# Performance work log

Measured on AMD Instinct MI355X. Metric: run time of the kernel, lower is better.

## Reference

```python
import jax, jax.numpy as jnp
import numpy as np


def _gcn_conv(h, src, dst, deg_inv_sqrt, W, b, num_nodes):
    # h: [N, Fin]; transform then normalized neighbor aggregation (incl. self-loops)
    h = h @ W  # [N, Fout]
    norm = deg_inv_sqrt[src] * deg_inv_sqrt[dst]  # [E+N]
    msgs = h[src] * norm[:, None]  # gather + scale
    out = jax.ops.segment_sum(msgs, dst, num_segments=num_nodes)
    return out + b


def setup_inputs() -> dict:
    key = jax.random.key(0)
    k1, k2, k3, k4 = jax.random.split(key, 4)
    N, E, F_IN, F_HID, F_OUT = 100000, 3200000, 1433, 16, 7
    x = jax.random.normal(k1, (N, F_IN), dtype=jnp.float32)
    edge_index = jax.random.randint(k2, (2, E), 0, N, dtype=jnp.int64)
    W1 = jax.random.normal(k3, (F_IN, F_HID), dtype=jnp.float32) * (1.0 / np.sqrt(F_IN))
    b1 = jnp.zeros((F_HID,), dtype=jnp.float32)
    W2 = jax.random.normal(k4, (F_HID, F_OUT), dtype=jnp.float32) * (1.0 / np.sqrt(F_HID))
    b2 = jnp.zeros((F_OUT,), dtype=jnp.float32)
    return {"x": x, "edge_index": edge_index, "W1": W1, "b1": b1, "W2": W2, "b2": b2}


def reference(x, edge_index, W1, b1, W2, b2):
    N = x.shape[0]
    # add self-loops (PyG GCNConv default)
    loops = jnp.arange(N, dtype=edge_index.dtype)
    src = jnp.concatenate([edge_index[0], loops])
    dst = jnp.concatenate([edge_index[1], loops])
    # symmetric normalization from in-degree over self-loop-augmented edges
    deg = jax.ops.segment_sum(jnp.ones_like(dst, dtype=x.dtype), dst, num_segments=N)
    deg_inv_sqrt = jnp.where(deg > 0, jax.lax.rsqrt(deg), 0.0)
    h = _gcn_conv(x, src, dst, deg_inv_sqrt, W1, b1, N)
    h = jax.nn.relu(h)
    # dropout is identity in eval mode (deterministic reference)
    h = _gcn_conv(h, src, dst, deg_inv_sqrt, W2, b2, N)
    return jax.nn.log_softmax(h, axis=1)
```

## Files before the change

kernel.cpp:

```cpp
#include <hip/hip_runtime.h>
#include <math.h>

#define F_IN 1433
#define F_HID 16
#define F_OUT 7
#define KSPLIT 8
#define KCHUNK 192
#define CAP 128
#define NSCAT 512

__device__ __forceinline__ unsigned short f2bf(float f) {
  unsigned u = __float_as_uint(f);
  u += 0x7fffu + ((u >> 16) & 1u);
  return (unsigned short)(u >> 16);
}

__device__ __forceinline__ unsigned pk2(float a, float b) {
  return (unsigned)f2bf(a) | ((unsigned)f2bf(b) << 16);
}

__device__ __forceinline__ void upk_add(unsigned u, float& lo, float& hi) {
  lo += __uint_as_float(u << 16);
  hi += __uint_as_float(u & 0xffff0000u);
}

__global__ __launch_bounds__(256) void k_zero(int* __restrict__ cnt, int N) {
  int i = blockIdx.x * 256 + threadIdx.x;
  if (i < N) cnt[i] = 0;
}

__global__ __launch_bounds__(256) void k_fused(
    const float* __restrict__ x, const float* __restrict__ W1,
    const int* __restrict__ src, const int* __restrict__ dst,
    int* __restrict__ cnt, int* __restrict__ csr, float* __restrict__ part,
    int N, int E, int nrb) {
  const int t = threadIdx.x;
  const int b = blockIdx.x;

  if (b < NSCAT) {
    const int ne4 = (E + 3) >> 2;
    for (int i4 = b * 256 + t; i4 < ne4; i4 += NSCAT * 256) {
      const int base = i4 * 4;
      if (base + 3 < E) {
        const int4 s = *(const int4*)(src + base);
        const int4 d = *(const int4*)(dst + base);
        int r;
        r = atomicAdd(&cnt[d.x], 1); csr[((size_t)d.x << 7) + r] = s.x;
        r = atomicAdd(&cnt[d.y], 1); csr[((size_t)d.y << 7) + r] = s.y;
        r = atomicAdd(&cnt[d.z], 1); csr[((size_t)d.z << 7) + r] = s.z;
        r = atomicAdd(&cnt[d.w], 1); csr[((size_t)d.w << 7) + r] = s.w;
      } else {
        for (int k = base; k < E; ++k) {
          const int d = dst[k];
          const int r = atomicAdd(&cnt[d], 1);
          csr[((size_t)d << 7) + r] = src[k];
        }
      }
    }
    return;
  }

  __shared__ float xs[256 * 33];
  const int g = b - NSCAT;
  const int chunk = g / nrb;
  const int rb = g - chunk * nrb;
  const int row0 = rb * 256;
  const int row = row0 + t;
  const int kk = t & 31;
  const int r0 = t >> 5;
  const int cbase = chunk * KCHUNK;
  const int kend = min(cbase + KCHUNK, F_IN);

  float acc[F_HID];
#pragma unroll
  for (int j = 0; j < F_HID; ++j) acc[j] = 0.0f;

  float reg[32];
  {
    const int k = cbase + kk;
    const bool kin = (k < kend);
#pragma unroll
    for (int i = 0; i < 32; ++i) {
      const int rg = row0 + r0 + 8 * i;
      reg[i] = (kin && rg < N) ? x[(size_t)rg * F_IN + k] : 0.0f;
    }
  }

  for (int k0 = cbase; k0 < kend; k0 += 32) {
#pragma unroll
    for (int i = 0; i < 32; ++i) xs[(r0 + 8 * i) * 33 + kk] = reg[i];
    __syncthreads();
    const int kn = k0 + 32;
    if (kn < kend) {
      const int k = kn + kk;
      const bool kin = (k < kend);
#pragma unroll
      for (int i = 0; i < 32; ++i) {
        const int rg = row0 + r0 + 8 * i;
        reg[i] = (kin && rg < N) ? x[(size_t)rg * F_IN + k] : 0.0f;
      }
    }
    const int kw = min(32, kend - k0);
    const float* __restrict__ wp = W1 + (size_t)k0 * F_HID;
    if (kw == 32) {
#pragma unroll
      for (int c = 0; c < 32; ++c) {
        const float xv = xs[t * 33 + c];
#pragma unroll
        for (int j = 0; j < F_HID; ++j)
          acc[j] = fmaf(xv, wp[c * F_HID + j], acc[j]);
      }
    } else {
      for (int c = 0; c < kw; ++c) {
        const float xv = xs[t * 33 + c];
#pragma unroll
        for (int j = 0; j < F_HID; ++j)
          acc[j] = fmaf(xv, wp[c * F_HID + j], acc[j]);
      }
    }
    __syncthreads();
  }

  if (row < N) {
    float4* __restrict__ pp =
        (float4*)(part + ((size_t)chunk * N + row) * F_HID);
    pp[0] = make_float4(acc[0], acc[1], acc[2], acc[3]);
    pp[1] = make_float4(acc[4], acc[5], acc[6], acc[7]);
    pp[2] = make_float4(acc[8], acc[9], acc[10], acc[11]);
    pp[3] = make_float4(acc[12], acc[13], acc[14], acc[15]);
  }
}

__global__ __launch_bounds__(256) void k_red(const float4* __restrict__ part,
                                             const int* __restrict__ cnt,
                                             uint2* __restrict__ h1b, int N) {
  const int idx = blockIdx.x * 256 + threadIdx.x;
  if (idx >= N * 4) return;
  const int row = idx >> 2;
  const size_t stride = (size_t)N * 4;
  float4 s = part[idx];
#pragma unroll
  for (int c = 1; c < KSPLIT; ++c) {
    const float4 p = part[c * stride + idx];
    s.x += p.x; s.y += p.y; s.z += p.z; s.w += p.w;
  }
  const float sc = rsqrtf((float)(cnt[row] + 1));
  uint2 o;
  o.x = pk2(s.x * sc, s.y * sc);
  o.y = pk2(s.z * sc, s.w * sc);
  h1b[idx] = o;
}

__device__ __forceinline__ void l1_finish(float a[8], int i, int d, int lane,
                                          int p, const uint4* __restrict__ h1v,
                                          const float* __restrict__ b1,
                                          const float* __restrict__ W2,
                                          uint4* __restrict__ h2v) {
#pragma unroll
  for (int m = 2; m <= 32; m <<= 1) {
#pragma unroll
    for (int j = 0; j < 8; ++j) a[j] += __shfl_xor(a[j], m);
  }
  const uint4 v = h1v[((size_t)i << 1) + p];
  upk_add(v.x, a[0], a[1]);
  upk_add(v.y, a[2], a[3]);
  upk_add(v.z, a[4], a[5]);
  upk_add(v.w, a[6], a[7]);
  const float sd = rsqrtf((float)(d + 1));
  const float4 bl = ((const float4*)b1)[p * 2];
  const float4 bh = ((const float4*)b1)[p * 2 + 1];
  float tt[8];
  tt[0] = fmaxf(fmaf(a[0], sd, bl.x), 0.f);
  tt[1] = fmaxf(fmaf(a[1], sd, bl.y), 0.f);
  tt[2] = fmaxf(fmaf(a[2], sd, bl.z), 0.f);
  tt[3] = fmaxf(fmaf(a[3], sd, bl.w), 0.f);
  tt[4] = fmaxf(fmaf(a[4], sd, bh.x), 0.f);
  tt[5] = fmaxf(fmaf(a[5], sd, bh.y), 0.f);
  tt[6] = fmaxf(fmaf(a[6], sd, bh.z), 0.f);
  tt[7] = fmaxf(fmaf(a[7], sd, bh.w), 0.f);
  const float* __restrict__ w = W2 + p * 8 * F_OUT;
  float o[F_OUT];
#pragma unroll
  for (int j = 0; j < F_OUT; ++j) {
    o[j] = tt[0] * w[0 * F_OUT + j] + tt[1] * w[1 * F_OUT + j] +
           tt[2] * w[2 * F_OUT + j] + tt[3] * w[3 * F_OUT + j] +
           tt[4] * w[4 * F_OUT + j] + tt[5] * w[5 * F_OUT + j] +
           tt[6] * w[6 * F_OUT + j] + tt[7] * w[7 * F_OUT + j];
  }
#pragma unroll
  for (int j = 0; j < F_OUT; ++j) o[j] += __shfl_xor(o[j], 1);
  if (lane == 0) {
    uint4 r;
    r.x = pk2(o[0] * sd, o[1] * sd);
    r.y = pk2(o[2] * sd, o[3] * sd);
    r.z = pk2(o[4] * sd, o[5] * sd);
    r.w = pk2(o[6] * sd, 0.0f);
    h2v[i] = r;
  }
}

__global__ __launch_bounds__(256) void k_agg1n(
    const int* __restrict__ cnt, const int* __restrict__ csr,
    const uint4* __restrict__ h1v, const float* __restrict__ b1,
    const float* __restrict__ W2, uint4* __restrict__ h2v, int N) {
  const int lane = threadIdx.x & 63;
  const int i0 = blockIdx.x * 8 + (threadIdx.x >> 6) * 2;
  if (i0 >= N) return;
  const int i1 = i0 + 1;
  const bool has1 = (i1 < N);
  const int nb = lane >> 1;
  const int p = lane & 1;

  const int d0 = cnt[i0];
  const int d1 = has1 ? cnt[i1] : 0;
  const int* __restrict__ row0 = csr + ((size_t)i0 << 7);
  const int* __restrict__ row1 = csr + ((size_t)i1 << 7);

  float A[8], B[8];
#pragma unroll
  for (int j = 0; j < 8; ++j) { A[j] = 0.f; B[j] = 0.f; }
  const int dm = max(d0, d1);
  for (int c0 = 0; c0 < dm; c0 += 32) {
    const int c = c0 + nb;
    if (c < d0) {
      const uint4 v = h1v[((size_t)row0[c] << 1) + p];
      upk_add(v.x, A[0], A[1]); upk_add(v.y, A[2], A[3]);
      upk_add(v.z, A[4], A[5]); upk_add(v.w, A[6], A[7]);
    }
    if (c < d1) {
      const uint4 v = h1v[((size_t)row1[c] << 1) + p];
      upk_add(v.x, B[0], B[1]); upk_add(v.y, B[2], B[3]);
      upk_add(v.z, B[4], B[5]); upk_add(v.w, B[6], B[7]);
    }
  }
  l1_finish(A, i0, d0, lane, p, h1v, b1, W2, h2v);
  if (has1) l1_finish(B, i1, d1, lane, p, h1v, b1, W2, h2v);
}

__device__ __forceinline__ void l2_finish(float a[8], int i, int d, int lane,
                                          const uint4* __restrict__ h2v,
                                          const float* __restrict__ b2,
                                          float* __restrict__ out) {
#pragma unroll
  for (int m = 1; m <= 32; m <<= 1) {
#pragma unroll
    for (int j = 0; j < 7; ++j) a[j] += __shfl_xor(a[j], m);
  }
  const uint4 v = h2v[i];
  upk_add(v.x, a[0], a[1]);
  upk_add(v.y, a[2], a[3]);
  upk_add(v.z, a[4], a[5]);
  float dummy = 0.f;
  upk_add(v.w, a[6], dummy);
  if (lane == 0) {
    const float sd = rsqrtf((float)(d + 1));
    float vv[7];
#pragma unroll
    for (int j = 0; j < 7; ++j) vv[j] = fmaf(a[j], sd, b2[j]);
    float m = fmaxf(fmaxf(fmaxf(vv[0], vv[1]), fmaxf(vv[2], vv[3])),
                    fmaxf(fmaxf(vv[4], vv[5]), vv[6]));
    float sum = 0.f;
#pragma unroll
    for (int j = 0; j < 7; ++j) sum += expf(vv[j] - m);
    const float l = m + logf(sum);
    float* __restrict__ op = out + (size_t)i * F_OUT;
#pragma unroll
    for (int j = 0; j < 7; ++j) op[j] = vv[j] - l;
  }
}

__global__ __launch_bounds__(256) void k_agg2n(const int* __restrict__ cnt,
                                               const int* __restrict__ csr,
                                               const uint4* __restrict__ h2v,
                                               const float* __restrict__ b2,
                                               float* __restrict__ out, int N) {
  const int lane = threadIdx.x & 63;
  const int i0 = blockIdx.x * 8 + (threadIdx.x >> 6) * 2;
  if (i0 >= N) return;
  const int i1 = i0 + 1;
  const bool has1 = (i1 < N);

  const int d0 = cnt[i0];
  const int d1 = has1 ? cnt[i1] : 0;
  const int* __restrict__ row0 = csr + ((size_t)i0 << 7);
  const int* __restrict__ row1 = csr + ((size_t)i1 << 7);

  float A[8], B[8];
#pragma unroll
  for (int j = 0; j < 8; ++j) { A[j] = 0.f; B[j] = 0.f; }
  const int dm = max(d0, d1);
  for (int c0 = 0; c0 < dm; c0 += 64) {
    const int c = c0 + lane;
    if (c < d0) {
      const uint4 v = h2v[row0[c]];
      upk_add(v.x, A[0], A[1]); upk_add(v.y, A[2], A[3]);
      upk_add(v.z, A[4], A[5]); upk_add(v.w, A[6], A[7]);
    }
    if (c < d1) {
      const uint4 v = h2v[row1[c]];
      upk_add(v.x, B[0], B[1]); upk_add(v.y, B[2], B[3]);
      upk_add(v.z, B[4], B[5]); upk_add(v.w, B[6], B[7]);
    }
  }
  l2_finish(A, i0, d0, lane, h2v, b2, out);
  if (has1) l2_finish(B, i1, d1, lane, h2v, b2, out);
}

extern "C" void kernel_launch(void* const* d_in, const int* in_sizes, int n_in,
                              void* d_out, int out_size, void* d_ws,
                              size_t ws_size, hipStream_t stream) {
  const float* x = (const float*)d_in[0];
  const int* ei = (const int*)d_in[1];
  const float* W1 = (const float*)d_in[2];
  const float* b1 = (const float*)d_in[3];
  const float* W2 = (const float*)d_in[4];
  const float* b2 = (const float*)d_in[5];

  const int N = in_sizes[0] / F_IN;
  const int E = in_sizes[1] / 2;
  const int* src = ei;
  const int* dst = ei + E;

  float* part = (float*)d_ws;
  unsigned short* h1b = (unsigned short*)(part + (size_t)KSPLIT * 16 * N);
  unsigned short* h2b = h1b + (size_t)16 * N;
  int* cnt = (int*)(h2b + (size_t)8 * N);
  int* csr = cnt + N;
  float* out = (float*)d_out;

  const int B = 256;
  const int nrb = (N + 255) / 256;

  k_zero<<<(N + B - 1) / B, B, 0, stream>>>(cnt, N);
  k_fused<<<NSCAT + nrb * KSPLIT, B, 0, stream>>>(x, W1, src, dst, cnt, csr,
                                                  part, N, E, nrb);
  k_red<<<(N * 4 + B - 1) / B, B, 0, stream>>>((const float4*)part, cnt,
                                               (uint2*)h1b, N);
  k_agg1n<<<(N + 7) / 8, B, 0, stream>>>(cnt, csr, (const uint4*)h1b, b1, W2,
                                         (uint4*)h2b, N);
  k_agg2n<<<(N + 7) / 8, B, 0, stream>>>(cnt, csr, (const uint4*)h2b, b2, out,
                                         N);
}
```

Baseline: 463.0 us.

## Compute first-layer GEMM with bf16 MFMA instead of split-K FMA

Replaces the shared-memory split-K fp32 FMA GEMM (x @ W1) with per-wave 16x16x32 bf16 MFMA tiles. Each wave reads x rows directly as float4 and converts them to bf16 on the fly. W1 is pre-packed into the MFMA B-operand layout in a prep kernel merged with the counter zeroing. This removes the split-K partial buffer and its reduction pass, leaving a single scale-and-pack kernel. The trade-off is that x is rounded to bf16 before the multiply, and the float4 loads land at unaligned row offsets.

```diff
diff --git a/kernel.cpp b/kernel.cpp
--- a/kernel.cpp
+++ b/kernel.cpp
@@ -4,10 +4,13 @@
 #define F_IN 1433
 #define F_HID 16
 #define F_OUT 7
-#define KSPLIT 8
-#define KCHUNK 192
 #define CAP 128
 #define NSCAT 512
+#define NKT 45
+#define KTFULL 44
+
+typedef __attribute__((ext_vector_type(8))) short bf16x8;
+typedef __attribute__((ext_vector_type(4))) float f32x4;
 
 __device__ __forceinline__ unsigned short f2bf(float f) {
   unsigned u = __float_as_uint(f);
@@ -24,16 +27,35 @@
   hi += __uint_as_float(u & 0xffff0000u);
 }
 
-__global__ __launch_bounds__(256) void k_zero(int* __restrict__ cnt, int N) {
-  int i = blockIdx.x * 256 + threadIdx.x;
-  if (i < N) cnt[i] = 0;
+__global__ __launch_bounds__(256) void k_prep(const float* __restrict__ W1,
+                                              int* __restrict__ cnt,
+                                              uint4* __restrict__ W1f, int N,
+                                              int nzb) {
+  const int b = blockIdx.x, t = threadIdx.x;
+  if (b < nzb) {
+    const int i = b * 256 + t;
+    if (i < N) cnt[i] = 0;
+    return;
+  }
+  if (t >= 64) return;
+  const int tile = b - nzb;
+  const int kg = t >> 4, n = t & 15;
+  unsigned u[4];
+#pragma unroll
+  for (int p = 0; p < 4; ++p) {
+    const int k0 = tile * 32 + kg * 8 + 2 * p;
+    const float a = (k0 < F_IN) ? W1[k0 * F_HID + n] : 0.0f;
+    const float bb = (k0 + 1 < F_IN) ? W1[(k0 + 1) * F_HID + n] : 0.0f;
+    u[p] = pk2(a, bb);
+  }
+  W1f[tile * 64 + t] = make_uint4(u[0], u[1], u[2], u[3]);
 }
 
 __global__ __launch_bounds__(256) void k_fused(
-    const float* __restrict__ x, const float* __restrict__ W1,
+    const float* __restrict__ x, const uint4* __restrict__ W1f,
     const int* __restrict__ src, const int* __restrict__ dst,
-    int* __restrict__ cnt, int* __restrict__ csr, float* __restrict__ part,
-    int N, int E, int nrb) {
+    int* __restrict__ cnt, int* __restrict__ csr, float* __restrict__ h1f,
+    int N, int E) {
   const int t = threadIdx.x;
   const int b = blockIdx.x;
 
@@ -60,95 +82,71 @@
     return;
   }
 
-  __shared__ float xs[256 * 33];
   const int g = b - NSCAT;
-  const int chunk = g / nrb;
-  const int rb = g - chunk * nrb;
-  const int row0 = rb * 256;
-  const int row = row0 + t;
-  const int kk = t & 31;
-  const int r0 = t >> 5;
-  const int cbase = chunk * KCHUNK;
-  const int kend = min(cbase + KCHUNK, F_IN);
-
-  float acc[F_HID];
-#pragma unroll
-  for (int j = 0; j < F_HID; ++j) acc[j] = 0.0f;
-
-  float reg[32];
+  const int w = t >> 6;
+  const int l = t & 63;
+  const int mtile = g * 4 + w;
+  const int row0 = mtile * 16;
+  if (row0 >= N) return;
+  const int m = l & 15;
+  const int kg = l >> 4;
+  int row = row0 + m;
+  if (row >= N) row = N - 1;
+  const float* __restrict__ xr = x + (size_t)row * F_IN;
+
+  f32x4 acc = {0.f, 0.f, 0.f, 0.f};
+  for (int kt = 0; kt < KTFULL; ++kt) {
+    const int k0 = kt * 32 + kg * 8;
+    const float4 xa = *(const float4*)(xr + k0);
+    const float4 xb = *(const float4*)(xr + k0 + 4);
+    union { unsigned u[4]; bf16x8 v; } av;
+    av.u[0] = pk2(xa.x, xa.y);
+    av.u[1] = pk2(xa.z, xa.w);
+    av.u[2] = pk2(xb.x, xb.y);
+    av.u[3] = pk2(xb.z, xb.w);
+    union { uint4 q; bf16x8 v; } wv;
+    wv.q = W1f[kt * 64 + l];
+    acc = __builtin_amdgcn_mfma_f32_16x16x32_bf16(av.v, wv.v, acc, 0, 0, 0);
+  }
   {
-    const int k = cbase + kk;
-    const bool kin = (k < kend);
-#pragma unroll
-    for (int i = 0; i < 32; ++i) {
-      const int rg = row0 + r0 + 8 * i;
-      reg[i] = (kin && rg < N) ? x[(size_t)rg * F_IN + k] : 0.0f;
-    }
-  }
-
-  for (int k0 = cbase; k0 < kend; k0 += 32) {
-#pragma unroll
-    for (int i = 0; i < 32; ++i) xs[(r0 + 8 * i) * 33 + kk] = reg[i];
-    __syncthreads();
-    const int kn = k0 + 32;
-    if (kn < kend) {
-      const int k = kn + kk;
-      const bool kin = (k < kend);
-#pragma unroll
-      for (int i = 0; i < 32; ++i) {
-        const int rg = row0 + r0 + 8 * i;
-        reg[i] = (kin && rg < N) ? x[(size_t)rg * F_IN + k] : 0.0f;
-      }
-    }
-    const int kw = min(32, kend - k0);
-    const float* __restrict__ wp = W1 + (size_t)k0 * F_HID;
-    if (kw == 32) {
-#pragma unroll
-      for (int c = 0; c < 32; ++c) {
-        const float xv = xs[t * 33 + c];
-#pragma unroll
-        for (int j = 0; j < F_HID; ++j)
-          acc[j] = fmaf(xv, wp[c * F_HID + j], acc[j]);
-      }
-    } else {
-      for (int c = 0; c < kw; ++c) {
-        const float xv = xs[t * 33 + c];
-#pragma unroll
-        for (int j = 0; j < F_HID; ++j)
-          acc[j] = fmaf(xv, wp[c * F_HID + j], acc[j]);
-      }
-    }
-    __syncthreads();
-  }
-
-  if (row < N) {
-    float4* __restrict__ pp =
-        (float4*)(part + ((size_t)chunk * N + row) * F_HID);
-    pp[0] = make_float4(acc[0], acc[1], acc[2], acc[3]);
-    pp[1] = make_float4(acc[4], acc[5], acc[6], acc[7]);
-    pp[2] = make_float4(acc[8], acc[9], acc[10], acc[11]);
-    pp[3] = make_float4(acc[12], acc[13], acc[14], acc[15]);
-  }
-}
-
-__global__ __launch_bounds__(256) void k_red(const float4* __restrict__ part,
-                                             const int* __restrict__ cnt,
-                                             uint2* __restrict__ h1b, int N) {
+    const int k0 = KTFULL * 32 + kg * 8;
+    float e[8];
+#pragma unroll
+    for (int j = 0; j < 8; ++j) {
+      const int k = k0 + j;
+      e[j] = (k < F_IN) ? xr[k] : 0.0f;
+    }
+    union { unsigned u[4]; bf16x8 v; } av;
+    av.u[0] = pk2(e[0], e[1]);
+    av.u[1] = pk2(e[2], e[3]);
+    av.u[2] = pk2(e[4], e[5]);
+    av.u[3] = pk2(e[6], e[7]);
+    union { uint4 q; bf16x8 v; } wv;
+    wv.q = W1f[KTFULL * 64 + l];
+    acc = __builtin_amdgcn_mfma_f32_16x16x32_bf16(av.v, wv.v, acc, 0, 0, 0);
+  }
+#pragma unroll
+  for (int r = 0; r < 4; ++r) {
+    const int orow = row0 + kg * 4 + r;
+    if (orow < N) h1f[(size_t)orow * F_HID + m] = acc[r];
+  }
+}
+
+__global__ __launch_bounds__(256) void k_scale(const float4* __restrict__ h1f,
+                                               const int* __restrict__ cnt,
+                                               uint4* __restrict__ h1v, int N) {
   const int idx = blockIdx.x * 256 + threadIdx.x;
-  if (idx >= N * 4) return;
-  const int row = idx >> 2;
-  const size_t stride = (size_t)N * 4;
-  float4 s = part[idx];
-#pragma unroll
-  for (int c = 1; c < KSPLIT; ++c) {
-    const float4 p = part[c * stride + idx];
-    s.x += p.x; s.y += p.y; s.z += p.z; s.w += p.w;
-  }
-  const float sc = rsqrtf((float)(cnt[row] + 1));
-  uint2 o;
-  o.x = pk2(s.x * sc, s.y * sc);
-  o.y = pk2(s.z * sc, s.w * sc);
-  h1b[idx] = o;
+  if (idx >= 2 * N) return;
+  const int node = idx >> 1;
+  const float sc = rsqrtf((float)(cnt[node] + 1));
+  const float4 a = h1f[idx * 2];
+  const float4 b = h1f[idx * 2 + 1];
+  uint4 o;
+  o.x = pk2(a.x * sc, a.y * sc);
+  o.y = pk2(a.z * sc, a.w * sc);
+  o.z = pk2(b.x * sc, b.y * sc);
+  o.w = pk2(b.z * sc, b.w * sc);
+  h1v[idx] = o;
 }
 
 __device__ __forceinline__ void l1_finish(float a[8], int i, int d, int lane,
@@ -321,21 +319,22 @@
   const int* src = ei;
   const int* dst = ei + E;
 
-  float* part = (float*)d_ws;
-  unsigned short* h1b = (unsigned short*)(part + (size_t)KSPLIT * 16 * N);
+  float* h1f = (float*)d_ws;
+  unsigned short* h1b = (unsigned short*)(h1f + (size_t)16 * N);
   unsigned short* h2b = h1b + (size_t)16 * N;
   int* cnt = (int*)(h2b + (size_t)8 * N);
   int* csr = cnt + N;
+  uint4* W1f = (uint4*)(csr + (size_t)N * CAP);
   float* out = (float*)d_out;
 
   const int B = 256;
-  const int nrb = (N + 255) / 256;
-
-  k_zero<<<(N + B - 1) / B, B, 0, stream>>>(cnt, N);
-  k_fused<<<NSCAT + nrb * KSPLIT, B, 0, stream>>>(x, W1, src, dst, cnt, csr,
-                                                  part, N, E, nrb);
-  k_red<<<(N * 4 + B - 1) / B, B, 0, stream>>>((const float4*)part, cnt,
-                                               (uint2*)h1b, N);
+  const int nzb = (N + B - 1) / B;
+  const int ngb = ((N + 15) / 16 + 3) / 4;
+
+  k_prep<<<nzb + NKT, B, 0, stream>>>(W1, cnt, W1f, N, nzb);
+  k_fused<<<NSCAT + ngb, B, 0, stream>>>(x, W1f, src, dst, cnt, csr, h1f, N, E);
+  k_scale<<<(2 * N + B - 1) / B, B, 0, stream>>>((const float4*)h1f, cnt,
+                                                 (uint4*)h1b, N);
   k_agg1n<<<(N + 7) / 8, B, 0, stream>>>(cnt, csr, (const uint4*)h1b, b1, W2,
                                          (uint4*)h2b, N);
   k_agg2n<<<(N + 7) / 8, B, 0, stream>>>(cnt, csr, (const uint4*)h2b, b2, out,
```

Result: faster. 410.3 us (-11.4%).
